# Kernel optimization log

Hardware: AMD Instinct MI355X
Metric: run time of the kernel (lower is better)

Reference implementation:

```python
import jax, jax.numpy as jnp
import numpy as np

NUM_HEADS = 16
HEAD_DIM = 64


def setup_inputs() -> dict:
    key = jax.random.key(0)
    k1, k2, k3 = jax.random.split(key, 3)
    dim = NUM_HEADS * HEAD_DIM  # 1024
    x = jax.random.normal(k1, (1, 4096, dim), dtype=jnp.float32)
    w_qkv = jax.random.normal(k2, (dim, 3 * dim), dtype=jnp.float32) * (dim ** -0.5)
    w_out = jax.random.normal(k3, (dim, dim), dtype=jnp.float32) * (dim ** -0.5)
    b_out = jnp.zeros((dim,), dtype=jnp.float32)
    return {"x": x, "w_qkv": w_qkv, "w_out": w_out, "b_out": b_out}


def reference(x, w_qkv, w_out, b_out):
    b, n, dim = x.shape
    h, d = NUM_HEADS, HEAD_DIM
    qkv = x @ w_qkv                                  # [b, n, 3*h*d]
    q, k, v = jnp.split(qkv, 3, axis=-1)
    q = q.reshape(b, n, h, d)
    k = k.reshape(b, n, h, d)
    v = v.reshape(b, n, h, d)  # NOTE: unused below — source module's bug uses K as V
    q = q * (d ** -0.5)
    # The chunked online-softmax in the source is mathematically exact softmax
    # attention; express it directly. Scores layout matches einsum '...qhd,...khd->...qhk'.
    scores = jnp.einsum('bqhd,bkhd->bqhk', q, k)     # [b, n, h, n]
    attn = jax.nn.softmax(scores, axis=-1)
    # Faithful to source bug: value_chunk was sliced from `key`, so V := K here.
    att = jnp.einsum('bqhk,bkhd->bqhd', attn, k)     # [b, n, h, d]
    out = att.reshape(b, n, h * d)
    return out @ w_out + b_out
```

## Files before the change

kernel.cpp:

```cpp
#include <hip/hip_runtime.h>
#include <hip/hip_bf16.h>

#define NT 4096
#define DIM 1024
#define NH 16
#define HD 64

typedef __attribute__((ext_vector_type(8))) short bf16x8;
typedef __attribute__((ext_vector_type(4))) float f32x4;
typedef __attribute__((ext_vector_type(16))) float f32x16;

__device__ __forceinline__ unsigned short f2b(float f) {
  union { float f; unsigned u; } v; v.f = f;
  unsigned r = v.u + 0x7fffu + ((v.u >> 16) & 1u);
  return (unsigned short)(r >> 16);
}
__device__ __forceinline__ float b2f(unsigned short u) {
  union { unsigned u; float f; } v; v.u = ((unsigned)u) << 16; return v.f;
}

__device__ __forceinline__ float fexp2(float x) {
#if __has_builtin(__builtin_amdgcn_exp2f)
  return __builtin_amdgcn_exp2f(x);
#else
  return exp2f(x);
#endif
}

__global__ void k_cvt(const float4* __restrict__ src, ushort4* __restrict__ dst, int n4) {
  int i = blockIdx.x * blockDim.x + threadIdx.x;
  if (i >= n4) return;
  float4 v = src[i];
  ushort4 o;
  o.x = f2b(v.x); o.y = f2b(v.y); o.z = f2b(v.z); o.w = f2b(v.w);
  dst[i] = o;
}

__global__ __launch_bounds__(256) void k_trans_w(const float* __restrict__ src, int S,
                                                 unsigned short* __restrict__ dst, int Kdim) {
  __shared__ float tile[32][33];
  int j0 = blockIdx.x * 32, k0 = blockIdx.y * 32;
  int t = threadIdx.x;
  int c = t & 31, rq = t >> 5;
#pragma unroll
  for (int i = 0; i < 4; i++) {
    int r = rq + i * 8;
    tile[r][c] = src[(size_t)(k0 + r) * S + j0 + c];
  }
  __syncthreads();
#pragma unroll
  for (int i = 0; i < 4; i++) {
    int jr = rq + i * 8;
    dst[(size_t)(j0 + jr) * Kdim + k0 + c] = f2b(tile[c][jr]);
  }
}

template <int EPI>
__global__ __launch_bounds__(256) void k_gemm(const unsigned short* __restrict__ A,
                                              const unsigned short* __restrict__ Bt,
                                              unsigned short* __restrict__ qh,
                                              unsigned short* __restrict__ krm,
                                              float* __restrict__ cout,
                                              const float* __restrict__ bias) {
  __shared__ unsigned short As[128][40];
  __shared__ unsigned short Bs[128][40];
  const int K = 1024;
  int m0 = blockIdx.y * 128, n0 = blockIdx.x * 128;
  int t = threadIdx.x;
  int w = t >> 6, l = t & 63;
  int wr = w >> 1, wc = w & 1;
  int lq = l & 15, lg = l >> 4;
  f32x4 zero = {0.f, 0.f, 0.f, 0.f};
  f32x4 acc[4][4];
#pragma unroll
  for (int i = 0; i < 4; i++)
#pragma unroll
    for (int j = 0; j < 4; j++) acc[i][j] = zero;

  for (int k0 = 0; k0 < K; k0 += 32) {
#pragma unroll
    for (int s = 0; s < 2; s++) {
      int slot = t + s * 256;
      int r = slot >> 2, c8 = (slot & 3) * 8;
      *reinterpret_cast<bf16x8*>(&As[r][c8]) =
          *reinterpret_cast<const bf16x8*>(A + (size_t)(m0 + r) * K + k0 + c8);
      *reinterpret_cast<bf16x8*>(&Bs[r][c8]) =
          *reinterpret_cast<const bf16x8*>(Bt + (size_t)(n0 + r) * K + k0 + c8);
    }
    __syncthreads();
    bf16x8 af[4], bf[4];
#pragma unroll
    for (int mi = 0; mi < 4; mi++)
      af[mi] = *reinterpret_cast<bf16x8*>(&As[wr * 64 + mi * 16 + lq][lg * 8]);
#pragma unroll
    for (int ni = 0; ni < 4; ni++)
      bf[ni] = *reinterpret_cast<bf16x8*>(&Bs[wc * 64 + ni * 16 + lq][lg * 8]);
#pragma unroll
    for (int mi = 0; mi < 4; mi++)
#pragma unroll
      for (int ni = 0; ni < 4; ni++)
        acc[mi][ni] =
            __builtin_amdgcn_mfma_f32_16x16x32_bf16(af[mi], bf[ni], acc[mi][ni], 0, 0, 0);
    __syncthreads();
  }
#pragma unroll
  for (int mi = 0; mi < 4; mi++) {
#pragma unroll
    for (int ni = 0; ni < 4; ni++) {
      int j = n0 + wc * 64 + ni * 16 + lq;
#pragma unroll
      for (int r = 0; r < 4; r++) {
        int row = m0 + wr * 64 + mi * 16 + lg * 4 + r;
        float v = acc[mi][ni][r];
        if (EPI == 0) {
          if (j < DIM) {
            qh[((size_t)(j >> 6) << 18) + (size_t)row * HD + (j & 63)] =
                f2b(v * 0.18033688011112042f);
          } else {
            int jj = j - DIM;
            krm[((size_t)(jj >> 6) << 18) + (size_t)row * HD + (jj & 63)] = f2b(v);
          }
        } else {
          cout[(size_t)row * DIM + j] = v + bias[j];
        }
      }
    }
  }
}

__global__ __launch_bounds__(256) void k_transK(const unsigned short* __restrict__ krm,
                                                unsigned short* __restrict__ kt) {
  __shared__ unsigned short tile[64][72];
  int h = blockIdx.y, n0 = blockIdx.x * 64;
  int t = threadIdx.x;
  const unsigned short* src = krm + (size_t)h * NT * HD;
#pragma unroll
  for (int s = 0; s < 2; s++) {
    int slot = t + s * 256;
    int r = slot >> 3, c8 = (slot & 7) * 8;
    *reinterpret_cast<bf16x8*>(&tile[r][c8]) =
        *reinterpret_cast<const bf16x8*>(src + (size_t)(n0 + r) * HD + c8);
  }
  __syncthreads();
  unsigned short* dst = kt + (size_t)h * HD * NT;
#pragma unroll
  for (int s = 0; s < 2; s++) {
    int slot = t + s * 256;
    int dd = slot & 63, c8 = (slot >> 6) * 8;
    bf16x8 vv;
#pragma unroll
    for (int i = 0; i < 8; i++) vv[i] = (short)tile[c8 + i][dd];
    *reinterpret_cast<bf16x8*>(dst + (size_t)dd * NT + n0 + c8) = vv;
  }
}

__global__ __launch_bounds__(256) void k_attn(const unsigned short* __restrict__ qh,
                                              const unsigned short* __restrict__ krm,
                                              const unsigned short* __restrict__ kt,
                                              unsigned short* __restrict__ part0,
                                              unsigned short* __restrict__ part1,
                                              float* __restrict__ stats) {
  __shared__ __align__(16) unsigned char sbuf[2][16384];

  int hw = blockIdx.x;
  int xcd = hw & 7, idx = hw >> 3;
  int h = xcd * 2 + (idx >> 6);
  int sub = idx & 63;
  int q0 = (sub & 31) * 128;
  int kvs = sub >> 5;
  int kv_base = kvs * (NT / 2);

  unsigned short* ob = kvs ? part1 : part0;
  float* mb = stats + (size_t)kvs * 2 * (NH * NT);
  float* lb = mb + NH * NT;

  int t = threadIdx.x, w = t >> 6, l = t & 63;
  int lq = l & 31, hi = l >> 5;
  const unsigned char* Kb = (const unsigned char*)(krm + (size_t)h * NT * HD);
  const unsigned char* Tb = (const unsigned char*)(kt + (size_t)h * HD * NT);
  const unsigned short* Qb = qh + (size_t)h * NT * HD;

  int qrow = q0 + w * 32 + lq;
  bf16x8 qf[4];
#pragma unroll
  for (int ds = 0; ds < 4; ds++)
    qf[ds] = *reinterpret_cast<const bf16x8*>(Qb + (size_t)qrow * HD + ds * 16 + hi * 8);

  int swz = (lq & 7) << 4;
  int qk_off[2][4], pv_off[2][4];
#pragma unroll
  for (int kb2 = 0; kb2 < 2; kb2++)
#pragma unroll
    for (int ds = 0; ds < 4; ds++)
      qk_off[kb2][ds] = ((kb2 * 32 + lq) << 7) + ((32 * ds + 16 * hi) ^ swz);
#pragma unroll
  for (int dblk = 0; dblk < 2; dblk++)
#pragma unroll
    for (int kb = 0; kb < 4; kb++)
      pv_off[dblk][kb] = 8192 + ((dblk * 32 + lq) << 7) + ((32 * kb + 16 * hi) ^ swz);

  f32x16 o0, o1;
#pragma unroll
  for (int r = 0; r < 16; r++) { o0[r] = 0.f; o1[r] = 0.f; }
  float m_run = -3.0e38f, l_run = 0.f;

  auto STAGE = [&](int b, int kv0) {
    unsigned char* base = &sbuf[b][0];
#pragma unroll
    for (int i = 0; i < 4; i++) {
      int c = w * 4 + i;
      int o = c * 1024 + l * 16;
      const unsigned char* g;
      if (c < 8) {
        int row = o >> 7;
        int so = (o ^ ((row & 7) << 4)) & 127;
        g = Kb + (size_t)(kv0 + row) * 128 + so;
      } else {
        int oo = o - 8192;
        int row = oo >> 7;
        int so = (oo ^ ((row & 7) << 4)) & 127;
        g = Tb + (size_t)row * 8192 + (size_t)kv0 * 2 + so;
      }
      __builtin_amdgcn_global_load_lds(
          (const __attribute__((address_space(1))) unsigned int*)g,
          (__attribute__((address_space(3))) unsigned int*)(base + c * 1024), 16, 0, 0);
    }
  };

  STAGE(0, kv_base);
  __syncthreads();

  for (int tile = 0; tile < 32; tile++) {
    int cur = tile & 1;
    if (tile < 31) STAGE(cur ^ 1, kv_base + (tile + 1) * 64);
    const unsigned char* KaB = &sbuf[cur][0];

    f32x16 s0, s1;
#pragma unroll
    for (int r = 0; r < 16; r++) { s0[r] = 0.f; s1[r] = 0.f; }
#pragma unroll
    for (int ds = 0; ds < 4; ds++) {
      bf16x8 a0 = *reinterpret_cast<const bf16x8*>(KaB + qk_off[0][ds]);
      bf16x8 a1 = *reinterpret_cast<const bf16x8*>(KaB + qk_off[1][ds]);
      s0 = __builtin_amdgcn_mfma_f32_32x32x16_bf16(a0, qf[ds], s0, 0, 0, 0);
      s1 = __builtin_amdgcn_mfma_f32_32x32x16_bf16(a1, qf[ds], s1, 0, 0, 0);
    }

    float pm = -3.0e38f;
#pragma unroll
    for (int r = 0; r < 16; r++) pm = fmaxf(pm, fmaxf(s0[r], s1[r]));
    pm = fmaxf(pm, __shfl_xor(pm, 32));
    if (__any(pm > m_run + 8.0f)) {
      float newm = fmaxf(m_run, pm);
      float al = fexp2(m_run - newm);
#pragma unroll
      for (int r = 0; r < 16; r++) {
        float av = __shfl(al, (r & 3) + 8 * (r >> 2) + 4 * hi);
        o0[r] *= av;
        o1[r] *= av;
      }
      l_run *= al;
      m_run = newm;
    }
    float p0[16], p1[16];
    float ps = 0.f;
#pragma unroll
    for (int r = 0; r < 16; r++) { p0[r] = fexp2(s0[r] - m_run); ps += p0[r]; }
#pragma unroll
    for (int r = 0; r < 16; r++) { p1[r] = fexp2(s1[r] - m_run); ps += p1[r]; }
    ps += __shfl_xor(ps, 32);
    l_run += ps;

    unsigned pk0[8], pk1[8];
#pragma unroll
    for (int i = 0; i < 8; i++) {
      asm("v_cvt_pk_bf16_f32 %0, %1, %2" : "=v"(pk0[i]) : "v"(p0[2 * i]), "v"(p0[2 * i + 1]));
      asm("v_cvt_pk_bf16_f32 %0, %1, %2" : "=v"(pk1[i]) : "v"(p1[2 * i]), "v"(p1[2 * i + 1]));
    }
    bf16x8 pf[4];
#pragma unroll
    for (int kb = 0; kb < 4; kb++) {
      const unsigned* pk = (kb < 2) ? pk0 : pk1;
      int m = kb & 1;
      unsigned d0 = pk[4 * m + 0], d1 = pk[4 * m + 1];
      unsigned e0 = pk[4 * m + 2], e1 = pk[4 * m + 3];
      asm volatile("v_permlane32_swap_b32 %0, %1" : "+v"(d0), "+v"(e0));
      asm volatile("v_permlane32_swap_b32 %0, %1" : "+v"(d1), "+v"(e1));
      union { unsigned u[4]; bf16x8 v; } uu;
      uu.u[0] = d0; uu.u[1] = d1; uu.u[2] = e0; uu.u[3] = e1;
      pf[kb] = uu.v;
    }

#pragma unroll
    for (int kb = 0; kb < 4; kb++) {
      bf16x8 v0 = *reinterpret_cast<const bf16x8*>(KaB + pv_off[0][kb]);
      o0 = __builtin_amdgcn_mfma_f32_32x32x16_bf16(pf[kb], v0, o0, 0, 0, 0);
    }
#pragma unroll
    for (int kb = 0; kb < 4; kb++) {
      bf16x8 v1 = *reinterpret_cast<const bf16x8*>(KaB + pv_off[1][kb]);
      o1 = __builtin_amdgcn_mfma_f32_32x32x16_bf16(pf[kb], v1, o1, 0, 0, 0);
    }
    __syncthreads();
  }

#pragma unroll
  for (int r = 0; r < 16; r++) {
    int qr = (r & 3) + 8 * (r >> 2) + 4 * hi;
    size_t grow = (size_t)(q0 + w * 32 + qr);
    ob[grow * DIM + h * HD + lq] = f2b(o0[r]);
    ob[grow * DIM + h * HD + 32 + lq] = f2b(o1[r]);
  }
  if (l < 32) {
    int q = q0 + w * 32 + lq;
    mb[h * NT + q] = m_run;
    lb[h * NT + q] = l_run;
  }
}

__global__ __launch_bounds__(256) void k_combine(unsigned short* __restrict__ p0b,
                                                 const unsigned short* __restrict__ p1b,
                                                 const float* __restrict__ stats) {
  int i = blockIdx.x * 256 + threadIdx.x;
  int base = i * 8;
  int q = base >> 10;
  int c = base & 1023;
  int h = c >> 6;
  const float* m0 = stats;
  const float* l0 = stats + NH * NT;
  const float* m1 = stats + 2 * NH * NT;
  const float* l1 = stats + 3 * NH * NT;
  float mm0 = m0[h * NT + q], ll0 = l0[h * NT + q];
  float mm1 = m1[h * NT + q], ll1 = l1[h * NT + q];
  float M = fmaxf(mm0, mm1);
  float s0 = fexp2(mm0 - M), s1 = fexp2(mm1 - M);
  float dn = ll0 * s0 + ll1 * s1;
  float a0 = s0 / dn, a1 = s1 / dn;
  bf16x8 v0 = *reinterpret_cast<const bf16x8*>(p0b + base);
  bf16x8 v1 = *reinterpret_cast<const bf16x8*>(p1b + base);
  bf16x8 o;
#pragma unroll
  for (int j = 0; j < 8; j++)
    o[j] = (short)f2b(b2f((unsigned short)v0[j]) * a0 + b2f((unsigned short)v1[j]) * a1);
  *reinterpret_cast<bf16x8*>(p0b + base) = o;
}

extern "C" void kernel_launch(void* const* d_in, const int* in_sizes, int n_in,
                              void* d_out, int out_size, void* d_ws, size_t ws_size,
                              hipStream_t stream) {
  const float* x = (const float*)d_in[0];
  const float* w_qkv = (const float*)d_in[1];
  const float* w_out = (const float*)d_in[2];
  const float* b_out = (const float*)d_in[3];
  float* out = (float*)d_out;

  char* ws = (char*)d_ws;
  unsigned short* xb   = (unsigned short*)(ws);
  unsigned short* wqkT = (unsigned short*)(ws + 8388608);
  unsigned short* woT  = (unsigned short*)(ws + 12582912);
  unsigned short* qhb  = (unsigned short*)(ws + 14680064);
  unsigned short* krm  = (unsigned short*)(ws + 23068672);
  unsigned short* ktb  = (unsigned short*)(ws + 31457280);
  unsigned short* attb = (unsigned short*)(ws + 39845888);
  float* stats = (float*)wqkT;

  k_cvt<<<(NT * DIM / 4 + 255) / 256, 256, 0, stream>>>((const float4*)x, (ushort4*)xb,
                                                        NT * DIM / 4);
  dim3 g1(2048 / 32, 1024 / 32);
  k_trans_w<<<g1, 256, 0, stream>>>(w_qkv, 3 * DIM, wqkT, DIM);
  dim3 g2(1024 / 32, 1024 / 32);
  k_trans_w<<<g2, 256, 0, stream>>>(w_out, DIM, woT, DIM);
  dim3 g3(2048 / 128, NT / 128);
  k_gemm<0><<<g3, 256, 0, stream>>>(xb, wqkT, qhb, krm, nullptr, nullptr);
  dim3 g4(NT / 64, NH);
  k_transK<<<g4, 256, 0, stream>>>(krm, ktb);
  k_attn<<<(NT / 128) * NH * 2, 256, 0, stream>>>(qhb, krm, ktb, attb, xb, stats);
  k_combine<<<NT * DIM / 8 / 256, 256, 0, stream>>>(attb, xb, stats);
  dim3 g5(DIM / 128, NT / 128);
  k_gemm<1><<<g5, 256, 0, stream>>>(attb, woT, nullptr, nullptr, out, b_out);
}
```

Before: 188.2 us.

## Relayout LDS tiles into chunk-major order and raise occupancy hint

Changes how K and K-transposed tiles are staged into LDS. The XOR-swizzled row layout becomes a chunk-major layout, so each lane's MFMA operand sits at a fixed base plus a constant offset, removing the per-lane offset arrays and their registers. It also sets a launch-bounds minimum of 4 blocks per CU and reuses the score registers for the exponentials to lower register pressure. The new layout changes the global access pattern (each lane reads 16 bytes from a different row) and may change LDS bank-conflict behaviour.

```diff
diff --git a/kernel.cpp b/kernel.cpp
--- a/kernel.cpp
+++ b/kernel.cpp
@@ -154,12 +154,12 @@
   }
 }
 
-__global__ __launch_bounds__(256) void k_attn(const unsigned short* __restrict__ qh,
-                                              const unsigned short* __restrict__ krm,
-                                              const unsigned short* __restrict__ kt,
-                                              unsigned short* __restrict__ part0,
-                                              unsigned short* __restrict__ part1,
-                                              float* __restrict__ stats) {
+__global__ __launch_bounds__(256, 4) void k_attn(const unsigned short* __restrict__ qh,
+                                                 const unsigned short* __restrict__ krm,
+                                                 const unsigned short* __restrict__ kt,
+                                                 unsigned short* __restrict__ part0,
+                                                 unsigned short* __restrict__ part1,
+                                                 float* __restrict__ stats) {
   __shared__ __align__(16) unsigned char sbuf[2][16384];
 
   int hw = blockIdx.x;
@@ -186,18 +186,7 @@
   for (int ds = 0; ds < 4; ds++)
     qf[ds] = *reinterpret_cast<const bf16x8*>(Qb + (size_t)qrow * HD + ds * 16 + hi * 8);
 
-  int swz = (lq & 7) << 4;
-  int qk_off[2][4], pv_off[2][4];
-#pragma unroll
-  for (int kb2 = 0; kb2 < 2; kb2++)
-#pragma unroll
-    for (int ds = 0; ds < 4; ds++)
-      qk_off[kb2][ds] = ((kb2 * 32 + lq) << 7) + ((32 * ds + 16 * hi) ^ swz);
-#pragma unroll
-  for (int dblk = 0; dblk < 2; dblk++)
-#pragma unroll
-    for (int kb = 0; kb < 4; kb++)
-      pv_off[dblk][kb] = 8192 + ((dblk * 32 + lq) << 7) + ((32 * kb + 16 * hi) ^ swz);
+  int rdbase = lq * 16 + hi * 1024;
 
   f32x16 o0, o1;
 #pragma unroll
@@ -209,17 +198,11 @@
 #pragma unroll
     for (int i = 0; i < 4; i++) {
       int c = w * 4 + i;
-      int o = c * 1024 + l * 16;
       const unsigned char* g;
       if (c < 8) {
-        int row = o >> 7;
-        int so = (o ^ ((row & 7) << 4)) & 127;
-        g = Kb + (size_t)(kv0 + row) * 128 + so;
+        g = Kb + (size_t)(kv0 + l) * 128 + (c >> 1) * 32 + (c & 1) * 16;
       } else {
-        int oo = o - 8192;
-        int row = oo >> 7;
-        int so = (oo ^ ((row & 7) << 4)) & 127;
-        g = Tb + (size_t)row * 8192 + (size_t)kv0 * 2 + so;
+        g = Tb + (size_t)l * 8192 + (size_t)kv0 * 2 + (c - 8) * 16;
       }
       __builtin_amdgcn_global_load_lds(
           (const __attribute__((address_space(1))) unsigned int*)g,
@@ -240,8 +223,8 @@
     for (int r = 0; r < 16; r++) { s0[r] = 0.f; s1[r] = 0.f; }
 #pragma unroll
     for (int ds = 0; ds < 4; ds++) {
-      bf16x8 a0 = *reinterpret_cast<const bf16x8*>(KaB + qk_off[0][ds]);
-      bf16x8 a1 = *reinterpret_cast<const bf16x8*>(KaB + qk_off[1][ds]);
+      bf16x8 a0 = *reinterpret_cast<const bf16x8*>(KaB + rdbase + ds * 2048);
+      bf16x8 a1 = *reinterpret_cast<const bf16x8*>(KaB + rdbase + ds * 2048 + 512);
       s0 = __builtin_amdgcn_mfma_f32_32x32x16_bf16(a0, qf[ds], s0, 0, 0, 0);
       s1 = __builtin_amdgcn_mfma_f32_32x32x16_bf16(a1, qf[ds], s1, 0, 0, 0);
     }
@@ -262,20 +245,19 @@
       l_run *= al;
       m_run = newm;
     }
-    float p0[16], p1[16];
     float ps = 0.f;
 #pragma unroll
-    for (int r = 0; r < 16; r++) { p0[r] = fexp2(s0[r] - m_run); ps += p0[r]; }
-#pragma unroll
-    for (int r = 0; r < 16; r++) { p1[r] = fexp2(s1[r] - m_run); ps += p1[r]; }
+    for (int r = 0; r < 16; r++) { s0[r] = fexp2(s0[r] - m_run); ps += s0[r]; }
+#pragma unroll
+    for (int r = 0; r < 16; r++) { s1[r] = fexp2(s1[r] - m_run); ps += s1[r]; }
     ps += __shfl_xor(ps, 32);
     l_run += ps;
 
     unsigned pk0[8], pk1[8];
 #pragma unroll
     for (int i = 0; i < 8; i++) {
-      asm("v_cvt_pk_bf16_f32 %0, %1, %2" : "=v"(pk0[i]) : "v"(p0[2 * i]), "v"(p0[2 * i + 1]));
-      asm("v_cvt_pk_bf16_f32 %0, %1, %2" : "=v"(pk1[i]) : "v"(p1[2 * i]), "v"(p1[2 * i + 1]));
+      asm("v_cvt_pk_bf16_f32 %0, %1, %2" : "=v"(pk0[i]) : "v"(s0[2 * i]), "v"(s0[2 * i + 1]));
+      asm("v_cvt_pk_bf16_f32 %0, %1, %2" : "=v"(pk1[i]) : "v"(s1[2 * i]), "v"(s1[2 * i + 1]));
     }
     bf16x8 pf[4];
 #pragma unroll
@@ -293,12 +275,12 @@
 
 #pragma unroll
     for (int kb = 0; kb < 4; kb++) {
-      bf16x8 v0 = *reinterpret_cast<const bf16x8*>(KaB + pv_off[0][kb]);
+      bf16x8 v0 = *reinterpret_cast<const bf16x8*>(KaB + rdbase + 8192 + kb * 2048);
       o0 = __builtin_amdgcn_mfma_f32_32x32x16_bf16(pf[kb], v0, o0, 0, 0, 0);
     }
 #pragma unroll
     for (int kb = 0; kb < 4; kb++) {
-      bf16x8 v1 = *reinterpret_cast<const bf16x8*>(KaB + pv_off[1][kb]);
+      bf16x8 v1 = *reinterpret_cast<const bf16x8*>(KaB + rdbase + 8192 + kb * 2048 + 512);
       o1 = __builtin_amdgcn_mfma_f32_32x32x16_bf16(pf[kb], v1, o1, 0, 0, 0);
     }
     __syncthreads();
```

After: 181.0 us. -3.8%, faster.
